# Performance work log

Hardware: AMD Instinct MI355X
Metric: run time of the kernel (lower is better)

The kernel has to match this reference:

```python
import jax, jax.numpy as jnp
import numpy as np

# SMPL-style 22-joint kinematic tree; parents[i] < i for i >= 2 as the module's loop requires.
PARENTS = np.array([-1, 0, 0, 0, 1, 2, 3, 4, 5, 6, 7, 8, 9, 9, 9, 12, 13, 14, 16, 17, 18, 19])
L, J, D6 = 65536, 22, 6


def cont6d_to_mat(d6):
    """6D continuous rotation -> 3x3 rotation matrix (Gram-Schmidt). Columns are b1,b2,b3."""
    a1, a2 = d6[..., :3], d6[..., 3:]
    b1 = a1 / jnp.maximum(jnp.linalg.norm(a1, axis=-1, keepdims=True), 1e-12)
    b2 = a2 - b1 * jnp.sum(b1 * a2, axis=-1, keepdims=True)
    b2 = b2 / jnp.maximum(jnp.linalg.norm(b2, axis=-1, keepdims=True), 1e-12)
    b3 = jnp.cross(b1, b2)
    return jnp.stack((b1, b2, b3), axis=-1)  # (..., 3, 3)


def setup_inputs() -> dict:
    key = jax.random.key(0)
    k1, k2 = jax.random.split(key)
    pred_series = jax.random.normal(k1, (L, J, D6), dtype=jnp.float32)
    offsets = 0.1 * jax.random.normal(k2, (J, 3), dtype=jnp.float32)  # bone offsets (buffer)
    return {"pred_series": pred_series, "offsets": offsets}


def reference(pred_series, offsets):
    # pred_series: (L, 22, 6) -> global positions (L, 22, 3)
    rot_mats = cont6d_to_mat(pred_series)          # (L, 22, 3, 3)

    # Cumulative root rotation: R_t = R_{t-1} @ delta_t, R_{-1} = I  (sequential scan over time)
    deltas = rot_mats[:, 1]                        # (L, 3, 3)
    def step(R, d):
        Rn = R @ d
        return Rn, Rn
    _, R = jax.lax.scan(step, jnp.eye(3, dtype=pred_series.dtype), deltas)  # (L, 3, 3)

    # Root translation: integrate rotated local velocities
    vel_local = pred_series[:, 0, :3]              # (L, 3)
    global_vel = jnp.einsum('tij,tj->ti', R, vel_local)
    root_pos = jnp.cumsum(global_vel, axis=0)      # (L, 3)

    # FK down the static tree, vectorized over time; unrolled over 22 joints (static).
    rots = [None] * J
    pos = [None] * J
    rots[0], pos[0] = R, root_pos
    rots[1] = R
    pos[1] = pos[0] + jnp.einsum('tij,j->ti', R, offsets[1])
    for i in range(2, J):
        p = int(PARENTS[i])
        rots[i] = jnp.einsum('tij,tjk->tik', rots[p], rot_mats[:, i])
        pos[i] = pos[p] + jnp.einsum('tij,j->ti', rots[p], offsets[i])
    return jnp.stack(pos, axis=1)                  # (L, 22, 3)
```

## Files before the change

kernel.cpp:

```cpp
#include <hip/hip_runtime.h>
#include <stdint.h>


#define LTOT 65536
#define ROW 132
#define P1B 256
#define NSCB (LTOT / P1B)

struct Aff { float A[9]; float b[3]; };

__device__ __forceinline__ void d6_to_mat(float a0, float a1, float a2,
                                          float a3, float a4, float a5,
                                          float R[9]) {
  float n1 = sqrtf(a0 * a0 + a1 * a1 + a2 * a2);
  float i1 = 1.0f / fmaxf(n1, 1e-12f);
  float b10 = a0 * i1, b11 = a1 * i1, b12 = a2 * i1;
  float d = b10 * a3 + b11 * a4 + b12 * a5;
  float c0 = a3 - d * b10, c1 = a4 - d * b11, c2 = a5 - d * b12;
  float n2 = sqrtf(c0 * c0 + c1 * c1 + c2 * c2);
  float i2 = 1.0f / fmaxf(n2, 1e-12f);
  float b20 = c0 * i2, b21 = c1 * i2, b22 = c2 * i2;
  float b30 = b11 * b22 - b12 * b21;
  float b31 = b12 * b20 - b10 * b22;
  float b32 = b10 * b21 - b11 * b20;
  R[0] = b10; R[1] = b20; R[2] = b30;
  R[3] = b11; R[4] = b21; R[5] = b31;
  R[6] = b12; R[7] = b22; R[8] = b32;
}

__device__ __forceinline__ void mat_mul(const float A[9], const float B[9], float C[9]) {
#pragma unroll
  for (int i = 0; i < 3; ++i)
#pragma unroll
    for (int j = 0; j < 3; ++j)
      C[i * 3 + j] = A[i * 3 + 0] * B[0 + j] + A[i * 3 + 1] * B[3 + j] + A[i * 3 + 2] * B[6 + j];
}

__device__ __forceinline__ void mat_vec(const float A[9], float x, float y, float z,
                                        float& ox, float& oy, float& oz) {
  ox = A[0] * x + A[1] * y + A[2] * z;
  oy = A[3] * x + A[4] * y + A[5] * z;
  oz = A[6] * x + A[7] * y + A[8] * z;
}

__device__ __forceinline__ void compose(const Aff& P, const Aff& T, Aff& O) {
  mat_mul(P.A, T.A, O.A);
  float bx, by, bz;
  mat_vec(P.A, T.b[0], T.b[1], T.b[2], bx, by, bz);
  O.b[0] = P.b[0] + bx; O.b[1] = P.b[1] + by; O.b[2] = P.b[2] + bz;
}

__device__ __forceinline__ void aff_identity(Aff& v) {
  v.A[0] = 1.f; v.A[1] = 0.f; v.A[2] = 0.f;
  v.A[3] = 0.f; v.A[4] = 1.f; v.A[5] = 0.f;
  v.A[6] = 0.f; v.A[7] = 0.f; v.A[8] = 1.f;
  v.b[0] = 0.f; v.b[1] = 0.f; v.b[2] = 0.f;
}

__device__ __forceinline__ void wave_scan(Aff& v, int lane) {
#pragma unroll
  for (int s = 1; s < 64; s <<= 1) {
    Aff u;
#pragma unroll
    for (int k = 0; k < 9; ++k) u.A[k] = __shfl_up(v.A[k], s, 64);
#pragma unroll
    for (int k = 0; k < 3; ++k) u.b[k] = __shfl_up(v.b[k], s, 64);
    if (lane >= s) { Aff t; compose(u, v, t); v = t; }
  }
}

__device__ __forceinline__ void block_scan(Aff& v, int lane, int wid,
                                           float (*sagg)[12], Aff& f) {
  wave_scan(v, lane);
  if (lane == 63) {
#pragma unroll
    for (int k = 0; k < 9; ++k) sagg[wid][k] = v.A[k];
#pragma unroll
    for (int k = 0; k < 3; ++k) sagg[wid][9 + k] = v.b[k];
  }
  __syncthreads();
  Aff pre; aff_identity(pre);
  for (int w = 0; w < wid; ++w) {
    Aff g, t2;
#pragma unroll
    for (int k = 0; k < 9; ++k) g.A[k] = sagg[w][k];
#pragma unroll
    for (int k = 0; k < 3; ++k) g.b[k] = sagg[w][9 + k];
    compose(pre, g, t2); pre = t2;
  }
  compose(pre, v, f);
}

__global__ __launch_bounds__(P1B) void fk_scan(const float* __restrict__ pred,
                                               float* __restrict__ loc,
                                               float* __restrict__ agg) {
  int tid = threadIdx.x;
  int t = blockIdx.x * P1B + tid;
  int lane = tid & 63, wid = tid >> 6;
  __shared__ float sagg[P1B / 64][12];

  const float4* q4 = (const float4*)(pred + (size_t)t * ROW);
  float4 qa = q4[0];
  float4 qb = q4[1];
  float4 qc = q4[2];
  Aff v;
  d6_to_mat(qb.z, qb.w, qc.x, qc.y, qc.z, qc.w, v.A);
  mat_vec(v.A, qa.x, qa.y, qa.z, v.b[0], v.b[1], v.b[2]);
  Aff f;
  block_scan(v, lane, wid, sagg, f);

  float4* o = (float4*)(loc + (size_t)t * 12);
  o[0] = make_float4(f.A[0], f.A[1], f.A[2], f.A[3]);
  o[1] = make_float4(f.A[4], f.A[5], f.A[6], f.A[7]);
  o[2] = make_float4(f.A[8], f.b[0], f.b[1], f.b[2]);
  if (tid == P1B - 1) {
    float4* a = (float4*)(agg + (size_t)blockIdx.x * 12);
    a[0] = make_float4(f.A[0], f.A[1], f.A[2], f.A[3]);
    a[1] = make_float4(f.A[4], f.A[5], f.A[6], f.A[7]);
    a[2] = make_float4(f.A[8], f.b[0], f.b[1], f.b[2]);
  }
}

__global__ __launch_bounds__(NSCB) void fk_scan2(const float* __restrict__ agg,
                                                 float* __restrict__ excl) {
  int i = threadIdx.x, lane = i & 63, wid = i >> 6;
  Aff v;
  {
    const float4* a = (const float4*)(agg + (size_t)i * 12);
    float4 a0 = a[0], a1 = a[1], a2 = a[2];
    v.A[0] = a0.x; v.A[1] = a0.y; v.A[2] = a0.z; v.A[3] = a0.w;
    v.A[4] = a1.x; v.A[5] = a1.y; v.A[6] = a1.z; v.A[7] = a1.w;
    v.A[8] = a2.x; v.b[0] = a2.y; v.b[1] = a2.z; v.b[2] = a2.w;
  }
  __shared__ float sagg[NSCB / 64][12];
  Aff f;
  block_scan(v, lane, wid, sagg, f);
  Aff pre; aff_identity(pre);
  for (int w = 0; w < wid; ++w) {
    Aff g, t2;
#pragma unroll
    for (int k = 0; k < 9; ++k) g.A[k] = sagg[w][k];
#pragma unroll
    for (int k = 0; k < 3; ++k) g.b[k] = sagg[w][9 + k];
    compose(pre, g, t2); pre = t2;
  }
  Aff e;
#pragma unroll
  for (int k = 0; k < 9; ++k) e.A[k] = __shfl_up(f.A[k], 1, 64);
#pragma unroll
  for (int k = 0; k < 3; ++k) e.b[k] = __shfl_up(f.b[k], 1, 64);
  if (lane == 0) e = pre;
  float4* o = (float4*)(excl + (size_t)i * 12);
  o[0] = make_float4(e.A[0], e.A[1], e.A[2], e.A[3]);
  o[1] = make_float4(e.A[4], e.A[5], e.A[6], e.A[7]);
  o[2] = make_float4(e.A[8], e.b[0], e.b[1], e.b[2]);
}

struct Rowv { float2 a, b, c; };
__device__ __forceinline__ Rowv loadrow(const float* q, int j) {
  const float2* p = (const float2*)(q + j * 6);
  Rowv r; r.a = p[0]; r.b = p[1]; r.c = p[2]; return r;
}
__device__ __forceinline__ void rowmat(const Rowv& r, float M[9]) {
  d6_to_mat(r.a.x, r.a.y, r.b.x, r.b.y, r.c.x, r.c.y, M);
}
__device__ __forceinline__ void childp(const float* Rp, const float* offs, int j,
                                       float px, float py, float pz,
                                       float& ox, float& oy, float& oz,
                                       float* ob) {
  float dx, dy, dz;
  mat_vec(Rp, offs[j * 3], offs[j * 3 + 1], offs[j * 3 + 2], dx, dy, dz);
  ox = px + dx; oy = py + dy; oz = pz + dz;
  ob[j * 3] = ox; ob[j * 3 + 1] = oy; ob[j * 3 + 2] = oz;
}

__global__ __launch_bounds__(320, 4) void fk_tree(const float* __restrict__ pred,
                                                  const float* __restrict__ offs,
                                                  const float* __restrict__ loc,
                                                  const float* __restrict__ excl,
                                                  float* __restrict__ out) {
  int lane = threadIdx.x;
  int chain = threadIdx.y;
  int t = blockIdx.x * 64 + lane;
  int sb = blockIdx.x >> 2;

  Aff e, l;
  {
    const float4* a = (const float4*)(excl + (size_t)sb * 12);
    float4 a0 = a[0], a1 = a[1], a2 = a[2];
    e.A[0] = a0.x; e.A[1] = a0.y; e.A[2] = a0.z; e.A[3] = a0.w;
    e.A[4] = a1.x; e.A[5] = a1.y; e.A[6] = a1.z; e.A[7] = a1.w;
    e.A[8] = a2.x; e.b[0] = a2.y; e.b[1] = a2.z; e.b[2] = a2.w;
  }
  {
    const float4* a = (const float4*)(loc + (size_t)t * 12);
    float4 a0 = a[0], a1 = a[1], a2 = a[2];
    l.A[0] = a0.x; l.A[1] = a0.y; l.A[2] = a0.z; l.A[3] = a0.w;
    l.A[4] = a1.x; l.A[5] = a1.y; l.A[6] = a1.z; l.A[7] = a1.w;
    l.A[8] = a2.x; l.b[0] = a2.y; l.b[1] = a2.z; l.b[2] = a2.w;
  }
  Aff g;
  compose(e, l, g);
  const float* R = g.A;
  float px = g.b[0], py = g.b[1], pz = g.b[2];
  const float* q = pred + (size_t)t * ROW;
  float* ob = out + (size_t)t * 66;

  float M[9], ra[9], rb[9];
  if (chain == 0) {
    Rowv w4 = loadrow(q, 4), w7 = loadrow(q, 7);
    ob[0] = px; ob[1] = py; ob[2] = pz;
    float p1x, p1y, p1z, p4x, p4y, p4z, p7x, p7y, p7z, dx, dy, dz;
    childp(R, offs, 1, px, py, pz, p1x, p1y, p1z, ob);
    rowmat(w4, M); mat_mul(R, M, ra);
    childp(R, offs, 4, p1x, p1y, p1z, p4x, p4y, p4z, ob);
    childp(ra, offs, 7, p4x, p4y, p4z, p7x, p7y, p7z, ob);
    rowmat(w7, M); mat_mul(ra, M, rb);
    childp(rb, offs, 10, p7x, p7y, p7z, dx, dy, dz, ob);
  } else if (chain == 1) {
    Rowv w2 = loadrow(q, 2), w5 = loadrow(q, 5), w8 = loadrow(q, 8);
    float p2x, p2y, p2z, p5x, p5y, p5z, p8x, p8y, p8z, dx, dy, dz;
    childp(R, offs, 2, px, py, pz, p2x, p2y, p2z, ob);
    rowmat(w2, M); mat_mul(R, M, ra);
    childp(ra, offs, 5, p2x, p2y, p2z, p5x, p5y, p5z, ob);
    rowmat(w5, M); mat_mul(ra, M, rb);
    childp(rb, offs, 8, p5x, p5y, p5z, p8x, p8y, p8z, ob);
    rowmat(w8, M); mat_mul(rb, M, ra);
    childp(ra, offs, 11, p8x, p8y, p8z, dx, dy, dz, ob);
  } else if (chain == 2) {
    Rowv w3 = loadrow(q, 3), w6 = loadrow(q, 6), w9 = loadrow(q, 9),
         w12 = loadrow(q, 12);
    float p3x, p3y, p3z, p6x, p6y, p6z, p9x, p9y, p9z;
    float p12x, p12y, p12z, dx, dy, dz;
    childp(R, offs, 3, px, py, pz, p3x, p3y, p3z, ob);
    rowmat(w3, M); mat_mul(R, M, ra);
    childp(ra, offs, 6, p3x, p3y, p3z, p6x, p6y, p6z, ob);
    rowmat(w6, M); mat_mul(ra, M, rb);
    childp(rb, offs, 9, p6x, p6y, p6z, p9x, p9y, p9z, ob);
    rowmat(w9, M); mat_mul(rb, M, ra);
    childp(ra, offs, 12, p9x, p9y, p9z, p12x, p12y, p12z, ob);
    rowmat(w12, M); mat_mul(ra, M, rb);
    childp(rb, offs, 15, p12x, p12y, p12z, dx, dy, dz, ob);
  } else {
    int jA = (chain == 3) ? 13 : 14;
    int jB = (chain == 3) ? 16 : 17;
    int jC = (chain == 3) ? 18 : 19;
    int jD = (chain == 3) ? 20 : 21;
    Rowv w3 = loadrow(q, 3), w6 = loadrow(q, 6), w9 = loadrow(q, 9);
    Rowv wA = loadrow(q, jA), wB = loadrow(q, jB), wC = loadrow(q, jC);
    float p3x, p3y, p3z, p6x, p6y, p6z, p9x, p9y, p9z;
    float pAx, pAy, pAz, pBx, pBy, pBz, pCx, pCy, pCz, dx, dy, dz;
    mat_vec(R, offs[9], offs[10], offs[11], dx, dy, dz);
    p3x = px + dx; p3y = py + dy; p3z = pz + dz;
    rowmat(w3, M); mat_mul(R, M, ra);
    mat_vec(ra, offs[18], offs[19], offs[20], dx, dy, dz);
    p6x = p3x + dx; p6y = p3y + dy; p6z = p3z + dz;
    rowmat(w6, M); mat_mul(ra, M, rb);
    mat_vec(rb, offs[27], offs[28], offs[29], dx, dy, dz);
    p9x = p6x + dx; p9y = p6y + dy; p9z = p6z + dz;
    rowmat(w9, M); mat_mul(rb, M, ra);
    childp(ra, offs, jA, p9x, p9y, p9z, pAx, pAy, pAz, ob);
    rowmat(wA, M); mat_mul(ra, M, rb);
    childp(rb, offs, jB, pAx, pAy, pAz, pBx, pBy, pBz, ob);
    rowmat(wB, M); mat_mul(rb, M, ra);
    childp(ra, offs, jC, pBx, pBy, pBz, pCx, pCy, pCz, ob);
    rowmat(wC, M); mat_mul(ra, M, rb);
    childp(rb, offs, jD, pCx, pCy, pCz, dx, dy, dz, ob);
  }
}

extern "C" void kernel_launch(void* const* d_in, const int* in_sizes, int n_in,
                              void* d_out, int out_size, void* d_ws, size_t ws_size,
                              hipStream_t stream) {
  const float* pred = (const float*)d_in[0];
  const float* offs = (const float*)d_in[1];
  float* out = (float*)d_out;

  float* ws = (float*)d_ws;
  float* loc  = ws;
  float* agg  = ws + (size_t)12 * LTOT;
  float* excl = ws + (size_t)12 * LTOT + 12 * NSCB;

  fk_scan<<<NSCB, P1B, 0, stream>>>(pred, loc, agg);
  fk_scan2<<<1, NSCB, 0, stream>>>(agg, excl);
  fk_tree<<<LTOT / 64, dim3(64, 5), 0, stream>>>(pred, offs, loc, excl, out);
}
```

Baseline: 105.5 us.

## Fuse scan passes into two kernels with redundant block-prefix recompute

Replaces the three-kernel scan-then-FK pipeline with two kernels. The first computes only per-block aggregates, and the second redoes the local scan, rescans all block aggregates in every block, and then runs the FK tree from shared memory. This removes the per-timestep local-transform round trip through global memory and one kernel launch. In exchange, each block redundantly scans 256 aggregates, the local scan runs twice, and the two hand chains are merged into one thread group with 4 chains per row instead of 5, which adds serial work and register pressure in the 1024-thread blocks.

After: 97.45 us. -7.7%, faster.

```diff
diff --git a/kernel.cpp b/kernel.cpp
--- a/kernel.cpp
+++ b/kernel.cpp
@@ -69,91 +69,48 @@
   }
 }
 
-__device__ __forceinline__ void block_scan(Aff& v, int lane, int wid,
-                                           float (*sagg)[12], Aff& f) {
-  wave_scan(v, lane);
-  if (lane == 63) {
-#pragma unroll
-    for (int k = 0; k < 9; ++k) sagg[wid][k] = v.A[k];
-#pragma unroll
-    for (int k = 0; k < 3; ++k) sagg[wid][9 + k] = v.b[k];
-  }
-  __syncthreads();
-  Aff pre; aff_identity(pre);
-  for (int w = 0; w < wid; ++w) {
-    Aff g, t2;
-#pragma unroll
-    for (int k = 0; k < 9; ++k) g.A[k] = sagg[w][k];
-#pragma unroll
-    for (int k = 0; k < 3; ++k) g.b[k] = sagg[w][9 + k];
-    compose(pre, g, t2); pre = t2;
-  }
-  compose(pre, v, f);
-}
-
-__global__ __launch_bounds__(P1B) void fk_scan(const float* __restrict__ pred,
-                                               float* __restrict__ loc,
-                                               float* __restrict__ agg) {
-  int tid = threadIdx.x;
-  int t = blockIdx.x * P1B + tid;
-  int lane = tid & 63, wid = tid >> 6;
-  __shared__ float sagg[P1B / 64][12];
-
+__device__ __forceinline__ void elem_transform(const float* __restrict__ pred,
+                                               int t, Aff& v) {
   const float4* q4 = (const float4*)(pred + (size_t)t * ROW);
   float4 qa = q4[0];
   float4 qb = q4[1];
   float4 qc = q4[2];
-  Aff v;
   d6_to_mat(qb.z, qb.w, qc.x, qc.y, qc.z, qc.w, v.A);
   mat_vec(v.A, qa.x, qa.y, qa.z, v.b[0], v.b[1], v.b[2]);
-  Aff f;
-  block_scan(v, lane, wid, sagg, f);
-
-  float4* o = (float4*)(loc + (size_t)t * 12);
-  o[0] = make_float4(f.A[0], f.A[1], f.A[2], f.A[3]);
-  o[1] = make_float4(f.A[4], f.A[5], f.A[6], f.A[7]);
-  o[2] = make_float4(f.A[8], f.b[0], f.b[1], f.b[2]);
+}
+
+__global__ __launch_bounds__(P1B) void fk_agg(const float* __restrict__ pred,
+                                              float* __restrict__ agg) {
+  int tid = threadIdx.x;
+  int t = blockIdx.x * P1B + tid;
+  int lane = tid & 63, wid = tid >> 6;
+  Aff v;
+  elem_transform(pred, t, v);
+  wave_scan(v, lane);
+  __shared__ float sagg[P1B / 64][12];
+  if (lane == 63) {
+#pragma unroll
+    for (int k = 0; k < 9; ++k) sagg[wid][k] = v.A[k];
+#pragma unroll
+    for (int k = 0; k < 3; ++k) sagg[wid][9 + k] = v.b[k];
+  }
+  __syncthreads();
   if (tid == P1B - 1) {
+    Aff pre; aff_identity(pre);
+    for (int w = 0; w < P1B / 64 - 1; ++w) {
+      Aff g, t2;
+#pragma unroll
+      for (int k = 0; k < 9; ++k) g.A[k] = sagg[w][k];
+#pragma unroll
+      for (int k = 0; k < 3; ++k) g.b[k] = sagg[w][9 + k];
+      compose(pre, g, t2); pre = t2;
+    }
+    Aff f; compose(pre, v, f);
     float4* a = (float4*)(agg + (size_t)blockIdx.x * 12);
     a[0] = make_float4(f.A[0], f.A[1], f.A[2], f.A[3]);
     a[1] = make_float4(f.A[4], f.A[5], f.A[6], f.A[7]);
     a[2] = make_float4(f.A[8], f.b[0], f.b[1], f.b[2]);
   }
-}
-
-__global__ __launch_bounds__(NSCB) void fk_scan2(const float* __restrict__ agg,
-                                                 float* __restrict__ excl) {
-  int i = threadIdx.x, lane = i & 63, wid = i >> 6;
-  Aff v;
-  {
-    const float4* a = (const float4*)(agg + (size_t)i * 12);
-    float4 a0 = a[0], a1 = a[1], a2 = a[2];
-    v.A[0] = a0.x; v.A[1] = a0.y; v.A[2] = a0.z; v.A[3] = a0.w;
-    v.A[4] = a1.x; v.A[5] = a1.y; v.A[6] = a1.z; v.A[7] = a1.w;
-    v.A[8] = a2.x; v.b[0] = a2.y; v.b[1] = a2.z; v.b[2] = a2.w;
-  }
-  __shared__ float sagg[NSCB / 64][12];
-  Aff f;
-  block_scan(v, lane, wid, sagg, f);
-  Aff pre; aff_identity(pre);
-  for (int w = 0; w < wid; ++w) {
-    Aff g, t2;
-#pragma unroll
-    for (int k = 0; k < 9; ++k) g.A[k] = sagg[w][k];
-#pragma unroll
-    for (int k = 0; k < 3; ++k) g.b[k] = sagg[w][9 + k];
-    compose(pre, g, t2); pre = t2;
-  }
-  Aff e;
-#pragma unroll
-  for (int k = 0; k < 9; ++k) e.A[k] = __shfl_up(f.A[k], 1, 64);
-#pragma unroll
-  for (int k = 0; k < 3; ++k) e.b[k] = __shfl_up(f.b[k], 1, 64);
-  if (lane == 0) e = pre;
-  float4* o = (float4*)(excl + (size_t)i * 12);
-  o[0] = make_float4(e.A[0], e.A[1], e.A[2], e.A[3]);
-  o[1] = make_float4(e.A[4], e.A[5], e.A[6], e.A[7]);
-  o[2] = make_float4(e.A[8], e.b[0], e.b[1], e.b[2]);
 }
 
 struct Rowv { float2 a, b, c; };
@@ -174,98 +131,180 @@
   ob[j * 3] = ox; ob[j * 3 + 1] = oy; ob[j * 3 + 2] = oz;
 }
 
-__global__ __launch_bounds__(320, 4) void fk_tree(const float* __restrict__ pred,
-                                                  const float* __restrict__ offs,
-                                                  const float* __restrict__ loc,
-                                                  const float* __restrict__ excl,
-                                                  float* __restrict__ out) {
-  int lane = threadIdx.x;
-  int chain = threadIdx.y;
-  int t = blockIdx.x * 64 + lane;
-  int sb = blockIdx.x >> 2;
-
-  Aff e, l;
-  {
-    const float4* a = (const float4*)(excl + (size_t)sb * 12);
-    float4 a0 = a[0], a1 = a[1], a2 = a[2];
-    e.A[0] = a0.x; e.A[1] = a0.y; e.A[2] = a0.z; e.A[3] = a0.w;
-    e.A[4] = a1.x; e.A[5] = a1.y; e.A[6] = a1.z; e.A[7] = a1.w;
-    e.A[8] = a2.x; e.b[0] = a2.y; e.b[1] = a2.z; e.b[2] = a2.w;
-  }
-  {
-    const float4* a = (const float4*)(loc + (size_t)t * 12);
-    float4 a0 = a[0], a1 = a[1], a2 = a[2];
-    l.A[0] = a0.x; l.A[1] = a0.y; l.A[2] = a0.z; l.A[3] = a0.w;
-    l.A[4] = a1.x; l.A[5] = a1.y; l.A[6] = a1.z; l.A[7] = a1.w;
-    l.A[8] = a2.x; l.b[0] = a2.y; l.b[1] = a2.z; l.b[2] = a2.w;
-  }
-  Aff g;
-  compose(e, l, g);
-  const float* R = g.A;
-  float px = g.b[0], py = g.b[1], pz = g.b[2];
+__global__ __launch_bounds__(1024) void fk_main(const float* __restrict__ pred,
+                                                const float* __restrict__ offs,
+                                                const float* __restrict__ agg,
+                                                float* __restrict__ out) {
+  int x = threadIdx.x;
+  int y = threadIdx.y;
+  int z = threadIdx.z;
+  int b = blockIdx.x;
+
+  __shared__ float sagg1[4][12];
+  __shared__ float sagg2[4][12];
+  __shared__ float ebuf[12];
+  __shared__ float sg[P1B][13];
+
+  int tl = z * 64 + x;
+  int t = b * P1B + tl;
   const float* q = pred + (size_t)t * ROW;
   float* ob = out + (size_t)t * 66;
 
+  Rowv w0, w1, w2, w3, w4, w5, w6, w7, w8;
+  if (y == 0) {
+    w0 = loadrow(q, 4); w1 = loadrow(q, 7);
+  } else if (y == 1) {
+    w0 = loadrow(q, 2); w1 = loadrow(q, 5); w2 = loadrow(q, 8);
+  } else if (y == 2) {
+    w0 = loadrow(q, 3); w1 = loadrow(q, 6); w2 = loadrow(q, 9);
+    w3 = loadrow(q, 12);
+  } else {
+    w0 = loadrow(q, 3); w1 = loadrow(q, 6); w2 = loadrow(q, 9);
+    w3 = loadrow(q, 13); w4 = loadrow(q, 16); w5 = loadrow(q, 18);
+    w6 = loadrow(q, 14); w7 = loadrow(q, 17); w8 = loadrow(q, 19);
+  }
+
+  int s = x + 64 * y;
+  Aff v, f;
+  Aff v2, incl;
+  if (z == 0) {
+    elem_transform(pred, b * P1B + s, v);
+    wave_scan(v, x);
+    if (x == 63) {
+#pragma unroll
+      for (int k = 0; k < 9; ++k) sagg1[y][k] = v.A[k];
+#pragma unroll
+      for (int k = 0; k < 3; ++k) sagg1[y][9 + k] = v.b[k];
+    }
+  } else if (z == 1) {
+    const float4* a = (const float4*)(agg + (size_t)s * 12);
+    float4 a0 = a[0], a1 = a[1], a2 = a[2];
+    v2.A[0] = a0.x; v2.A[1] = a0.y; v2.A[2] = a0.z; v2.A[3] = a0.w;
+    v2.A[4] = a1.x; v2.A[5] = a1.y; v2.A[6] = a1.z; v2.A[7] = a1.w;
+    v2.A[8] = a2.x; v2.b[0] = a2.y; v2.b[1] = a2.z; v2.b[2] = a2.w;
+    wave_scan(v2, x);
+    if (x == 63) {
+#pragma unroll
+      for (int k = 0; k < 9; ++k) sagg2[y][k] = v2.A[k];
+#pragma unroll
+      for (int k = 0; k < 3; ++k) sagg2[y][9 + k] = v2.b[k];
+    }
+  }
+  __syncthreads();
+
+  if (z == 0) {
+    Aff pre; aff_identity(pre);
+    for (int w = 0; w < y; ++w) {
+      Aff gg, t2;
+#pragma unroll
+      for (int k = 0; k < 9; ++k) gg.A[k] = sagg1[w][k];
+#pragma unroll
+      for (int k = 0; k < 3; ++k) gg.b[k] = sagg1[w][9 + k];
+      compose(pre, gg, t2); pre = t2;
+    }
+    compose(pre, v, f);
+  } else if (z == 1) {
+    Aff pre; aff_identity(pre);
+    for (int w = 0; w < y; ++w) {
+      Aff gg, t2;
+#pragma unroll
+      for (int k = 0; k < 9; ++k) gg.A[k] = sagg2[w][k];
+#pragma unroll
+      for (int k = 0; k < 3; ++k) gg.b[k] = sagg2[w][9 + k];
+      compose(pre, gg, t2); pre = t2;
+    }
+    compose(pre, v2, incl);
+    if (s == b - 1) {
+#pragma unroll
+      for (int k = 0; k < 9; ++k) ebuf[k] = incl.A[k];
+#pragma unroll
+      for (int k = 0; k < 3; ++k) ebuf[9 + k] = incl.b[k];
+    }
+  }
+  __syncthreads();
+
+  if (z == 0) {
+    Aff eb;
+    if (b == 0) aff_identity(eb);
+    else {
+#pragma unroll
+      for (int k = 0; k < 9; ++k) eb.A[k] = ebuf[k];
+#pragma unroll
+      for (int k = 0; k < 3; ++k) eb.b[k] = ebuf[9 + k];
+    }
+    Aff g; compose(eb, f, g);
+#pragma unroll
+    for (int k = 0; k < 9; ++k) sg[s][k] = g.A[k];
+#pragma unroll
+    for (int k = 0; k < 3; ++k) sg[s][9 + k] = g.b[k];
+  }
+  __syncthreads();
+
+  float R[9];
+#pragma unroll
+  for (int k = 0; k < 9; ++k) R[k] = sg[tl][k];
+  float px = sg[tl][9], py = sg[tl][10], pz = sg[tl][11];
+
   float M[9], ra[9], rb[9];
-  if (chain == 0) {
-    Rowv w4 = loadrow(q, 4), w7 = loadrow(q, 7);
+  if (y == 0) {
     ob[0] = px; ob[1] = py; ob[2] = pz;
     float p1x, p1y, p1z, p4x, p4y, p4z, p7x, p7y, p7z, dx, dy, dz;
     childp(R, offs, 1, px, py, pz, p1x, p1y, p1z, ob);
-    rowmat(w4, M); mat_mul(R, M, ra);
     childp(R, offs, 4, p1x, p1y, p1z, p4x, p4y, p4z, ob);
+    rowmat(w0, M); mat_mul(R, M, ra);
     childp(ra, offs, 7, p4x, p4y, p4z, p7x, p7y, p7z, ob);
-    rowmat(w7, M); mat_mul(ra, M, rb);
+    rowmat(w1, M); mat_mul(ra, M, rb);
     childp(rb, offs, 10, p7x, p7y, p7z, dx, dy, dz, ob);
-  } else if (chain == 1) {
-    Rowv w2 = loadrow(q, 2), w5 = loadrow(q, 5), w8 = loadrow(q, 8);
+  } else if (y == 1) {
     float p2x, p2y, p2z, p5x, p5y, p5z, p8x, p8y, p8z, dx, dy, dz;
     childp(R, offs, 2, px, py, pz, p2x, p2y, p2z, ob);
-    rowmat(w2, M); mat_mul(R, M, ra);
+    rowmat(w0, M); mat_mul(R, M, ra);
     childp(ra, offs, 5, p2x, p2y, p2z, p5x, p5y, p5z, ob);
-    rowmat(w5, M); mat_mul(ra, M, rb);
+    rowmat(w1, M); mat_mul(ra, M, rb);
     childp(rb, offs, 8, p5x, p5y, p5z, p8x, p8y, p8z, ob);
-    rowmat(w8, M); mat_mul(rb, M, ra);
+    rowmat(w2, M); mat_mul(rb, M, ra);
     childp(ra, offs, 11, p8x, p8y, p8z, dx, dy, dz, ob);
-  } else if (chain == 2) {
-    Rowv w3 = loadrow(q, 3), w6 = loadrow(q, 6), w9 = loadrow(q, 9),
-         w12 = loadrow(q, 12);
+  } else if (y == 2) {
     float p3x, p3y, p3z, p6x, p6y, p6z, p9x, p9y, p9z;
     float p12x, p12y, p12z, dx, dy, dz;
     childp(R, offs, 3, px, py, pz, p3x, p3y, p3z, ob);
-    rowmat(w3, M); mat_mul(R, M, ra);
+    rowmat(w0, M); mat_mul(R, M, ra);
     childp(ra, offs, 6, p3x, p3y, p3z, p6x, p6y, p6z, ob);
-    rowmat(w6, M); mat_mul(ra, M, rb);
+    rowmat(w1, M); mat_mul(ra, M, rb);
     childp(rb, offs, 9, p6x, p6y, p6z, p9x, p9y, p9z, ob);
-    rowmat(w9, M); mat_mul(rb, M, ra);
+    rowmat(w2, M); mat_mul(rb, M, ra);
     childp(ra, offs, 12, p9x, p9y, p9z, p12x, p12y, p12z, ob);
-    rowmat(w12, M); mat_mul(ra, M, rb);
+    rowmat(w3, M); mat_mul(ra, M, rb);
     childp(rb, offs, 15, p12x, p12y, p12z, dx, dy, dz, ob);
   } else {
-    int jA = (chain == 3) ? 13 : 14;
-    int jB = (chain == 3) ? 16 : 17;
-    int jC = (chain == 3) ? 18 : 19;
-    int jD = (chain == 3) ? 20 : 21;
-    Rowv w3 = loadrow(q, 3), w6 = loadrow(q, 6), w9 = loadrow(q, 9);
-    Rowv wA = loadrow(q, jA), wB = loadrow(q, jB), wC = loadrow(q, jC);
-    float p3x, p3y, p3z, p6x, p6y, p6z, p9x, p9y, p9z;
-    float pAx, pAy, pAz, pBx, pBy, pBz, pCx, pCy, pCz, dx, dy, dz;
+    float p3x, p3y, p3z, p6x, p6y, p6z, p9x, p9y, p9z, dx, dy, dz;
     mat_vec(R, offs[9], offs[10], offs[11], dx, dy, dz);
     p3x = px + dx; p3y = py + dy; p3z = pz + dz;
-    rowmat(w3, M); mat_mul(R, M, ra);
+    rowmat(w0, M); mat_mul(R, M, ra);
     mat_vec(ra, offs[18], offs[19], offs[20], dx, dy, dz);
     p6x = p3x + dx; p6y = p3y + dy; p6z = p3z + dz;
-    rowmat(w6, M); mat_mul(ra, M, rb);
+    rowmat(w1, M); mat_mul(ra, M, rb);
     mat_vec(rb, offs[27], offs[28], offs[29], dx, dy, dz);
     p9x = p6x + dx; p9y = p6y + dy; p9z = p6z + dz;
-    rowmat(w9, M); mat_mul(rb, M, ra);
-    childp(ra, offs, jA, p9x, p9y, p9z, pAx, pAy, pAz, ob);
-    rowmat(wA, M); mat_mul(ra, M, rb);
-    childp(rb, offs, jB, pAx, pAy, pAz, pBx, pBy, pBz, ob);
-    rowmat(wB, M); mat_mul(rb, M, ra);
-    childp(ra, offs, jC, pBx, pBy, pBz, pCx, pCy, pCz, ob);
-    rowmat(wC, M); mat_mul(ra, M, rb);
-    childp(rb, offs, jD, pCx, pCy, pCz, dx, dy, dz, ob);
+    rowmat(w2, M); mat_mul(rb, M, ra);
+    float r9s[9];
+#pragma unroll
+    for (int k = 0; k < 9; ++k) r9s[k] = ra[k];
+    float pAx, pAy, pAz, pBx, pBy, pBz, pCx, pCy, pCz;
+    childp(r9s, offs, 13, p9x, p9y, p9z, pAx, pAy, pAz, ob);
+    rowmat(w3, M); mat_mul(r9s, M, rb);
+    childp(rb, offs, 16, pAx, pAy, pAz, pBx, pBy, pBz, ob);
+    rowmat(w4, M); mat_mul(rb, M, ra);
+    childp(ra, offs, 18, pBx, pBy, pBz, pCx, pCy, pCz, ob);
+    rowmat(w5, M); mat_mul(ra, M, rb);
+    childp(rb, offs, 20, pCx, pCy, pCz, dx, dy, dz, ob);
+    childp(r9s, offs, 14, p9x, p9y, p9z, pAx, pAy, pAz, ob);
+    rowmat(w6, M); mat_mul(r9s, M, rb);
+    childp(rb, offs, 17, pAx, pAy, pAz, pBx, pBy, pBz, ob);
+    rowmat(w7, M); mat_mul(rb, M, ra);
+    childp(ra, offs, 19, pBx, pBy, pBz, pCx, pCy, pCz, ob);
+    rowmat(w8, M); mat_mul(ra, M, rb);
+    childp(rb, offs, 21, pCx, pCy, pCz, dx, dy, dz, ob);
   }
 }
 
@@ -275,13 +314,8 @@
   const float* pred = (const float*)d_in[0];
   const float* offs = (const float*)d_in[1];
   float* out = (float*)d_out;
-
-  float* ws = (float*)d_ws;
-  float* loc  = ws;
-  float* agg  = ws + (size_t)12 * LTOT;
-  float* excl = ws + (size_t)12 * LTOT + 12 * NSCB;
-
-  fk_scan<<<NSCB, P1B, 0, stream>>>(pred, loc, agg);
-  fk_scan2<<<1, NSCB, 0, stream>>>(agg, excl);
-  fk_tree<<<LTOT / 64, dim3(64, 5), 0, stream>>>(pred, offs, loc, excl, out);
-}
+  float* agg = (float*)d_ws;
+
+  fk_agg<<<NSCB, P1B, 0, stream>>>(pred, agg);
+  fk_main<<<NSCB, dim3(64, 4, 4), 0, stream>>>(pred, offs, agg, out);
+}
```
